# Optimization experiments

Hardware: AMD Instinct MI355X
Metric: run time of the kernel (lower is better)

The kernel has to match this reference:

```python
import jax, jax.numpy as jnp
import numpy as np

N = 32       # number of variables (per-var LSTMs)
L = 128      # window length
D = 128      # hidden dim
HEADS = 8
TAU_MAX = 5
ALPHA = 0.7  # attn_decay_alpha
B = 128      # number of time-ordered windows


def setup_inputs() -> dict:
    key = jax.random.key(0)
    ks = jax.random.split(key, 20)
    s = 0.1
    f = lambda k, shape: (jax.random.normal(k, shape, jnp.float32) * s)
    return {
        "X": jax.random.normal(ks[0], (B, L, N), jnp.float32),
        # per-variable encoder LSTM (input size 1): W_ih (N,4D), W_hh (N,4D,D), combined-style biases kept separate
        "enc_Wih": f(ks[1], (N, 4 * D)),
        "enc_Whh": f(ks[2], (N, 4 * D, D)),
        "enc_b": f(ks[3], (N, 4 * D)),            # b_ih + b_hh merged (mathematically identical)
        "pool_w": f(ks[4], (N, D)),
        "pool_b": f(ks[5], (N,)),
        # shared MultiheadAttention params (torch layout: in_proj (3D,D))
        "in_proj_w": f(ks[6], (3 * D, D)),
        "in_proj_b": f(ks[7], (3 * D,)),
        "out_proj_w": f(ks[8], (D, D)),
        "out_proj_b": f(ks[9], (D,)),
        # per-variable decoder: init_h/init_c Linear(d,d), LSTM(1,d) (input is all-zeros so W_ih drops out), out Linear(d,1)
        "dec_initH_w": f(ks[10], (N, D, D)),
        "dec_initH_b": f(ks[11], (N, D)),
        "dec_initC_w": f(ks[12], (N, D, D)),
        "dec_initC_b": f(ks[13], (N, D)),
        "dec_Whh": f(ks[14], (N, 4 * D, D)),
        "dec_bih": f(ks[15], (N, 4 * D)),
        "dec_bhh": f(ks[16], (N, 4 * D)),
        "dec_out_w": f(ks[17], (N, D)),
        "dec_out_b": f(ks[18], (N,)),
    }


def _lstm_cell(gates, c):
    # torch gate order: i, f, g, o
    i, fg, g, o = jnp.split(gates, 4, axis=-1)
    i = jax.nn.sigmoid(i); fg = jax.nn.sigmoid(fg)
    g = jnp.tanh(g); o = jax.nn.sigmoid(o)
    c = fg * c + i * g
    h = o * jnp.tanh(c)
    return h, c


def _encode(X, Wih, Whh, b, pool_w, pool_b):
    # X: (B,L,N); encoder consumes first L-1 steps of each variable, batched over all N vars
    x = jnp.transpose(X[:, :-1, :], (1, 2, 0))  # (T, N, B)
    Bn = X.shape[0]
    h0 = jnp.zeros((N, Bn, D), X.dtype)

    def step(carry, x_t):  # x_t: (N,B)
        h, c = carry
        gates = (x_t[..., None] * Wih[:, None, :]
                 + jnp.einsum('nbd,ngd->nbg', h, Whh)
                 + b[:, None, :])
        h, c = _lstm_cell(gates, c)
        return (h, c), h

    _, H = jax.lax.scan(step, (h0, h0), x)  # H: (T,N,B,D)
    # TemporalAttnPool: softmax over time of a linear score, weighted sum
    scores = jnp.einsum('tnbd,nd->tnb', H, pool_w) + pool_b[None, :, None]
    a = jax.nn.softmax(scores, axis=0)
    C = jnp.einsum('tnb,tnbd->bnd', a, H)  # (B,N,D)
    return C


def _mha(Q, KV, in_w, in_b, out_w, out_b):
    dh = D // HEADS
    q = Q @ in_w[:D].T + in_b[:D]
    k = KV @ in_w[D:2 * D].T + in_b[D:2 * D]
    v = KV @ in_w[2 * D:].T + in_b[2 * D:]
    sp = lambda x: x.reshape(x.shape[0], x.shape[1], HEADS, dh)
    q, k, v = sp(q), sp(k), sp(v)
    scores = jnp.einsum('bqhd,bkhd->bhqk', q, k) / float(np.sqrt(dh))
    attn = jax.nn.softmax(scores, axis=-1)
    o = jnp.einsum('bhqk,bkhd->bqhd', attn, v).reshape(Q.shape)
    return o @ out_w.T + out_b


def _cross_attend(C, in_w, in_b, out_w, out_b):
    Bn = C.shape[0]
    tmax = min(TAU_MAX, Bn - 1)
    if tmax <= 0:
        return C
    out_sum = jnp.zeros_like(C)
    w_sum = jnp.zeros((Bn, 1, 1), C.dtype)
    for tau in range(1, tmax + 1):  # small fixed loop over lags
        o = _mha(C[tau:], C[:-tau], in_w, in_b, out_w, out_b)
        w = float(np.exp(-ALPHA * (tau - 1)))  # attn_agg == 'decay'
        out_sum = out_sum.at[tau:].add(o * w)
        w_sum = w_sum.at[tau:].add(w)
    out = out_sum / jnp.clip(w_sum, 1e-8)
    return C + out  # residual=True


def _decode(C_star, iHw, iHb, iCw, iCb, Whh, bih, bhh, ow, ob):
    # h0/c0 from tanh(Linear(c_star)); LSTM input is all-zeros so input term reduces to b_ih
    h0 = jnp.tanh(jnp.einsum('bnd,ned->nbe', C_star, iHw) + iHb[:, None, :])
    c0 = jnp.tanh(jnp.einsum('bnd,ned->nbe', C_star, iCw) + iCb[:, None, :])
    b = (bih + bhh)[:, None, :]  # (N,1,4D)

    def step(carry, _):
        h, c = carry
        gates = jnp.einsum('nbd,ngd->nbg', h, Whh) + b
        h, c = _lstm_cell(gates, c)
        o = jnp.einsum('nbd,nd->nb', h, ow) + ob[:, None]
        return (h, c), o

    _, O = jax.lax.scan(step, (h0, c0), None, length=L)  # (L,N,B)
    recon = jnp.transpose(O[:L - 1], (2, 0, 1))  # (B,L-1,N)
    pred = O[L - 1].T                            # (B,N)
    return recon, pred


def reference(X, enc_Wih, enc_Whh, enc_b, pool_w, pool_b,
              in_proj_w, in_proj_b, out_proj_w, out_proj_b,
              dec_initH_w, dec_initH_b, dec_initC_w, dec_initC_b,
              dec_Whh, dec_bih, dec_bhh, dec_out_w, dec_out_b):
    C = _encode(X, enc_Wih, enc_Whh, enc_b, pool_w, pool_b)
    C_star = _cross_attend(C, in_proj_w, in_proj_b, out_proj_w, out_proj_b)
    recon, pred = _decode(C_star, dec_initH_w, dec_initH_b, dec_initC_w, dec_initC_b,
                          dec_Whh, dec_bih, dec_bhh, dec_out_w, dec_out_b)
    return recon, pred, C_star
```

## Files before the change

kernel.cpp:

```cpp
#include <hip/hip_runtime.h>
#include <hip/hip_bf16.h>

typedef unsigned short ushort_t;
typedef unsigned int uint_t;

#define DD   128
#define G4   512
#define BT   16
#define NB   128
#define NV   32

#define OFF_WIH   0
#define OFF_EB    16384
#define OFF_PW    32768
#define OFF_PB    36864
#define OFF_INW   37120
#define OFF_INB   86272
#define OFF_OUTW  86784
#define OFF_OUTB  103168
#define OFF_IHB   103424
#define OFF_ICB   107520
#define OFF_DBIH  111616
#define OFF_DBHH  128000
#define OFF_DOW   144384
#define OFF_DOB   148480
#define P_TOTAL   148736
#define OFF_FLAGS (OFF_PB + 32)

typedef __attribute__((ext_vector_type(8))) short bf16x8;
typedef __attribute__((ext_vector_type(4))) float f32x4;

__device__ __forceinline__ float bf2f(ushort_t u) {
    union { uint_t i; float f; } x; x.i = ((uint_t)u) << 16; return x.f;
}
__device__ __forceinline__ ushort_t f2bf(float f) {
    __hip_bfloat16 h = __float2bfloat16(f);
    return *(ushort_t*)&h;
}
__device__ __forceinline__ uint_t f2u(float f) {
    union { float f; uint_t i; } x; x.f = f; return x.i;
}
__device__ __forceinline__ float u2f(uint_t u) {
    union { uint_t i; float f; } x; x.i = u; return x.f;
}
__device__ __forceinline__ float exp2_f(float x) {
    float r; asm("v_exp_f32 %0, %1" : "=v"(r) : "v"(x)); return r;
}
__device__ __forceinline__ float sigmoid_f(float x) {
    return __builtin_amdgcn_rcpf(1.f + exp2_f(x * -1.442695041f));
}
__device__ __forceinline__ float tanh_f(float x) {
    return 1.f - 2.f * __builtin_amdgcn_rcpf(exp2_f(x * 2.885390082f) + 1.f);
}
__device__ __forceinline__ uint_t cvt_pk_bf16(float a, float b) {
    uint_t r; asm("v_cvt_pk_bf16_f32 %0, %1, %2" : "=v"(r) : "v"(a), "v"(b)); return r;
}
__device__ __forceinline__ bf16x8 pack8(f32x4 a, f32x4 b) {
    union { uint_t u[4]; bf16x8 v; } x;
    x.u[0] = cvt_pk_bf16(a.x, a.y); x.u[1] = cvt_pk_bf16(a.z, a.w);
    x.u[2] = cvt_pk_bf16(b.x, b.y); x.u[3] = cvt_pk_bf16(b.z, b.w);
    return x.v;
}
__device__ __forceinline__ float swz_bcast_l15(float v) {
    return u2f((uint_t)__builtin_amdgcn_ds_swizzle((int)f2u(v), 0x000F));
}
__device__ __forceinline__ void store_out(void* out, long idx, float v, int bf) {
    if (bf) ((ushort_t*)out)[idx] = f2bf(v);
    else    ((float*)out)[idx]    = v;
}
#define LBAR() do { asm volatile("s_waitcnt lgkmcnt(0)" ::: "memory"); \
                    __builtin_amdgcn_s_barrier(); } while (0)

__device__ __forceinline__ int wave_probe(const void* p, int elems) {
    int cap = elems < 2048 ? elems : 2048;
    int lane = threadIdx.x & 63;
    const ushort_t* u = (const ushort_t*)p;
    int cnt = 0, tot = 0;
    for (int j = lane; j < cap; j += 64) {
        ushort_t x = u[j];
        float af = fabsf(bf2f(x));
        tot++;
        if (x == 0 || (af > 1e-7f && af < 100.f)) cnt++;
    }
    #pragma unroll
    for (int off = 32; off >= 1; off >>= 1) {
        cnt += __shfl_xor(cnt, off);
        tot += __shfl_xor(tot, off);
    }
    return (cnt * 10 >= tot * 9) ? 1 : 0;
}

struct Ptr19 { const void* p[19]; };

__global__ __launch_bounds__(256) void prep_kernel(Ptr19 a, float* __restrict__ P,
                                                   float* __restrict__ Xc) {
    __shared__ float tile[32][65];
    if (blockIdx.x < 581) {
        int base = blockIdx.x * 256;
        int src, o0, size;
        if      (base < OFF_EB)   { src = 1;  o0 = base - OFF_WIH;  size = 16384; }
        else if (base < OFF_PW)   { src = 3;  o0 = base - OFF_EB;   size = 16384; }
        else if (base < OFF_PB)   { src = 4;  o0 = base - OFF_PW;   size = 4096;  }
        else if (base < OFF_INW)  { src = 5;  o0 = base - OFF_PB;   size = 32;    }
        else if (base < OFF_INB)  { src = 6;  o0 = base - OFF_INW;  size = 49152; }
        else if (base < OFF_OUTW) { src = 7;  o0 = base - OFF_INB;  size = 384;   }
        else if (base < OFF_OUTB) { src = 8;  o0 = base - OFF_OUTW; size = 16384; }
        else if (base < OFF_IHB)  { src = 9;  o0 = base - OFF_OUTB; size = 128;   }
        else if (base < OFF_ICB)  { src = 11; o0 = base - OFF_IHB;  size = 4096;  }
        else if (base < OFF_DBIH) { src = 13; o0 = base - OFF_ICB;  size = 4096;  }
        else if (base < OFF_DBHH) { src = 15; o0 = base - OFF_DBIH; size = 16384; }
        else if (base < OFF_DOW)  { src = 16; o0 = base - OFF_DBHH; size = 16384; }
        else if (base < OFF_DOB)  { src = 17; o0 = base - OFF_DOW;  size = 4096;  }
        else                      { src = 18; o0 = base - OFF_DOB;  size = 32;    }
        int bf = wave_probe(a.p[src], size);
        int off = o0 + (int)threadIdx.x;
        if (off < size)
            P[base + threadIdx.x] = bf ? bf2f(((const ushort_t*)a.p[src])[off])
                                       : ((const float*)a.p[src])[off];
    } else if (blockIdx.x < 837) {
        int bf = wave_probe(a.p[0], 2048);
        int idx2 = blockIdx.x - 581;
        int bt = (idx2 & 3) * 32, tn0 = (idx2 >> 2) * 64;
        const void* src = a.p[0];
        int tx = threadIdx.x & 63, ty = threadIdx.x >> 6;
        #pragma unroll
        for (int k = 0; k < 8; k++) {
            int row = ty * 8 + k;
            int idx = (bt + row) * 4096 + tn0 + tx;
            tile[row][tx] = bf ? bf2f(((const ushort_t*)src)[idx]) : ((const float*)src)[idx];
        }
        __syncthreads();
        int bx = threadIdx.x & 31, tyy = threadIdx.x >> 5;
        #pragma unroll
        for (int k = 0; k < 8; k++) {
            int tn = tn0 + tyy * 8 + k;
            int t = tn >> 5, nn = tn & 31;
            Xc[t * 4096 + nn * 128 + bt + bx] = tile[bx][tyy * 8 + k];
        }
    } else {
        int which = blockIdx.x - 837;
        int src = (which == 0) ? 0 : (which == 1) ? 2 : (which == 2) ? 10
                : (which == 3) ? 12 : 14;
        int flag = wave_probe(a.p[src], 2048);
        if (threadIdx.x == 0) P[OFF_FLAGS + which] = (float)flag;
    }
}

__global__ __launch_bounds__(512, 2) void enc_kernel(
    const float* __restrict__ Xc, const void* __restrict__ Wraw,
    const float* __restrict__ P, float* __restrict__ Cout)
{
    const int n = blockIdx.y, b0 = blockIdx.x * BT;
    const int tid = threadIdx.x;
    const int w = tid >> 6, lane = tid & 63;
    const int l15 = lane & 15, quad = lane >> 4;
    const int wbf = P[OFF_FLAGS + 1] > 0.5f;
    const int bown = b0 + l15;

    __shared__ alignas(16) ushort_t hS[2][16 * 136];
    for (int i = tid; i < 16 * 136; i += 512) hS[0][i] = 0;

    bf16x8 afrag[4][4];
    #pragma unroll
    for (int typ = 0; typ < 4; typ++) {
        const int g = typ * 128 + 16 * w + l15;
        #pragma unroll
        for (int kc = 0; kc < 4; kc++) {
            const int base = (n * G4 + g) * DD + 32 * kc + 8 * quad;
            if (wbf) {
                afrag[typ][kc] = *(const bf16x8*)((const ushort_t*)Wraw + base);
            } else {
                const float* fp = (const float*)Wraw + base;
                afrag[typ][kc] = pack8(*(const f32x4*)fp, *(const f32x4*)(fp + 4));
            }
        }
    }

    bf16x8 pfrag[4];
    #pragma unroll
    for (int kc = 0; kc < 4; kc++) {
        bf16x8 tmp;
        #pragma unroll
        for (int j = 0; j < 8; j++)
            tmp[j] = (l15 == 0 || l15 == 8)
                   ? (short)f2bf(P[OFF_PW + n * DD + 32 * kc + 8 * quad + j]) : (short)0;
        pfrag[kc] = tmp;
    }

    f32x4 bias4[4], wih4[4];
    #pragma unroll
    for (int typ = 0; typ < 4; typ++) {
        int base = n * G4 + typ * 128 + 16 * w + 4 * quad;
        bias4[typ] = *(const f32x4*)&P[OFF_EB + base];
        wih4[typ]  = *(const f32x4*)&P[OFF_WIH + base];
    }
    const float pb_r = P[OFF_PB + n];
    const f32x4 pb4 = {pb_r, pb_r, pb_r, pb_r};

    float cst[4] = {0.f, 0.f, 0.f, 0.f};
    f32x4 hprev  = {0.f, 0.f, 0.f, 0.f};
    f32x4 hprev2 = {0.f, 0.f, 0.f, 0.f};
    f32x4 Cacc   = {0.f, 0.f, 0.f, 0.f};
    float lR = 0.f, pend = 0.f;

    const float* xnext = Xc + n * 128 + bown;
    float xq = *xnext;
    xnext += 4096;

    if (w & 4) __builtin_amdgcn_s_setprio(1);

#define ENC_STEP(T, RB)                                                              \
    do {                                                                             \
        LBAR();                                                                      \
        bf16x8 bh[4];                                                                \
        _Pragma("unroll")                                                            \
        for (int kc = 0; kc < 4; kc++)                                               \
            bh[kc] = *(const bf16x8*)&hS[RB][l15 * 136 + 32 * kc + 8 * quad];        \
        if ((T) >= 2) {     \
            float e = __expf(pend);                                                  \
            lR += e;                                                                 \
            f32x4 ev = {e, e, e, e};                                                 \
            Cacc += ev * hprev2;                                                     \
        }                                                                            \
        f32x4 xv = {xq, xq, xq, xq};                                                 \
        f32x4 acc[4];                                                                \
        _Pragma("unroll")                                                            \
        for (int typ = 0; typ < 4; typ++)                                            \
            acc[typ] = __builtin_amdgcn_mfma_f32_16x16x32_bf16(                      \
                afrag[typ][0], bh[0], bias4[typ] + xv * wih4[typ], 0, 0, 0);         \
        f32x4 accP = __builtin_amdgcn_mfma_f32_16x16x32_bf16(pfrag[0], bh[0], pb4, 0, 0, 0); \
        xq = *xnext; xnext += 4096;    \
        _Pragma("unroll")                                                            \
        for (int kc = 1; kc < 4; kc++) {                                             \
            accP = __builtin_amdgcn_mfma_f32_16x16x32_bf16(pfrag[kc], bh[kc], accP, 0, 0, 0); \
            _Pragma("unroll")                                                        \
            for (int typ = 0; typ < 4; typ++)                                        \
                acc[typ] = __builtin_amdgcn_mfma_f32_16x16x32_bf16(afrag[typ][kc], bh[kc], acc[typ], 0, 0, 0); \
        }                                                                            \
        if ((T) >= 1) pend = swz_bcast_l15(accP[0]);   \
        float hh[4];                                                                 \
        _Pragma("unroll")                                                            \
        for (int r = 0; r < 4; r++) {                                                \
            float ii = sigmoid_f(acc[0][r]);                                         \
            float ff = sigmoid_f(acc[1][r]);                                         \
            float g2 = tanh_f(acc[2][r]);                                            \
            float oo = sigmoid_f(acc[3][r]);                                         \
            float cc = ff * cst[r] + ii * g2;                                        \
            cst[r] = cc;                                                             \
            hh[r] = oo * tanh_f(cc);                                                 \
        }                                                                            \
        hprev2 = hprev;                                                              \
        hprev.x = hh[0]; hprev.y = hh[1]; hprev.z = hh[2]; hprev.w = hh[3];          \
        uint2 hw;                                                                    \
        hw.x = cvt_pk_bf16(hh[0], hh[1]);                                            \
        hw.y = cvt_pk_bf16(hh[2], hh[3]);                                            \
        *(uint2*)&hS[(RB) ^ 1][l15 * 136 + 16 * w + 4 * quad] = hw;                  \
    } while (0)

    for (int tp = 0; tp < 63; tp++) {
        ENC_STEP(2 * tp, 0);
        ENC_STEP(2 * tp + 1, 1);
    }
    ENC_STEP(126, 0);
#undef ENC_STEP

    LBAR();
    {
        float e = __expf(pend);
        lR += e;
        f32x4 ev = {e, e, e, e};
        Cacc += ev * hprev2;

        f32x4 accP = __builtin_amdgcn_mfma_f32_16x16x32_bf16(
            pfrag[0], *(const bf16x8*)&hS[1][l15 * 136 + 8 * quad], pb4, 0, 0, 0);
        #pragma unroll
        for (int kc = 1; kc < 4; kc++) {
            bf16x8 bh = *(const bf16x8*)&hS[1][l15 * 136 + 32 * kc + 8 * quad];
            accP = __builtin_amdgcn_mfma_f32_16x16x32_bf16(pfrag[kc], bh, accP, 0, 0, 0);
        }
        float e2 = __expf(swz_bcast_l15(accP[0]));
        lR += e2;
        f32x4 ev2 = {e2, e2, e2, e2};
        Cacc += ev2 * hprev;
    }
    float inv = 1.f / lR;
    f32x4 iv = {inv, inv, inv, inv};
    f32x4 cv = Cacc * iv;
    *(f32x4*)&Cout[bown * (NV * DD) + n * DD + 16 * w + 4 * quad] = cv;
}

__global__ __launch_bounds__(256) void qkv_kernel(
    const float* __restrict__ C, const float* __restrict__ P,
    float* __restrict__ q, float* __restrict__ k, float* __restrict__ v)
{
    int b = blockIdx.x, p = blockIdx.y, tid = threadIdx.x;
    int j = tid & 127, half = tid >> 7;
    __shared__ float Cb[NV * DD];
    for (int i = tid; i < NV * DD; i += 256) Cb[i] = C[b * (NV * DD) + i];
    __syncthreads();

    const float* wrow = P + OFF_INW + (p * DD + j) * DD;
    float bias = P[OFF_INB + p * DD + j];
    float acc[16];
    #pragma unroll
    for (int nn = 0; nn < 16; nn++) acc[nn] = bias;

    for (int dc = 0; dc < DD; dc += 8) {
        float4 w0 = *(const float4*)&wrow[dc];
        float4 w1 = *(const float4*)&wrow[dc + 4];
        #pragma unroll
        for (int nn = 0; nn < 16; nn++) {
            const float* cb = &Cb[(half * 16 + nn) * DD + dc];
            float4 c0 = *(float4*)&cb[0];
            float4 c1 = *(float4*)&cb[4];
            acc[nn] += c0.x * w0.x + c0.y * w0.y + c0.z * w0.z + c0.w * w0.w
                     + c1.x * w1.x + c1.y * w1.y + c1.z * w1.z + c1.w * w1.w;
        }
    }
    float* dst = (p == 0) ? q : (p == 1) ? k : v;
    for (int nn = 0; nn < 16; nn++)
        dst[b * (NV * DD) + (half * 16 + nn) * DD + j] = acc[nn];
}

__global__ __launch_bounds__(128) void attn_kernel(
    const float* __restrict__ q, const float* __restrict__ k, const float* __restrict__ v,
    const float* __restrict__ C, const float* __restrict__ P,
    float* __restrict__ Cstar, void* __restrict__ dout)
{
    int b = blockIdx.x, half = blockIdx.y, tid = threadIdx.x;
    int obf = P[OFF_FLAGS + 0] > 0.5f;
    int n0 = half * 16;
    __shared__ float Qs[16 * DD], Ks[NV * DD], Vs[NV * DD];
    float* Os = Ks;
    for (int i = tid; i < 16 * DD; i += 128) Qs[i] = q[b * (NV * DD) + n0 * DD + i];
    __syncthreads();

    int hh = tid >> 4, qi = tid & 15;
    float qreg[16];
    #pragma unroll
    for (int u = 0; u < 4; u++) {
        float4 t4 = *(float4*)&Qs[qi * DD + hh * 16 + 4 * u];
        qreg[4*u] = t4.x; qreg[4*u+1] = t4.y; qreg[4*u+2] = t4.z; qreg[4*u+3] = t4.w;
    }

    float Oacc[16];
    #pragma unroll
    for (int u = 0; u < 16; u++) Oacc[u] = 0.f;
    float wsum = 0.f;
    int tmax = (b < 5) ? b : 5;

    for (int tau = 1; tau <= tmax; tau++) {
        __syncthreads();
        for (int i = tid; i < NV * DD; i += 128) {
            Ks[i] = k[(b - tau) * (NV * DD) + i];
            Vs[i] = v[(b - tau) * (NV * DD) + i];
        }
        __syncthreads();

        float s[NV];
        #pragma unroll
        for (int kk = 0; kk < NV; kk++) {
            float a = 0.f;
            #pragma unroll
            for (int u = 0; u < 4; u++) {
                float4 kv = *(float4*)&Ks[kk * DD + hh * 16 + 4 * u];
                a += qreg[4*u] * kv.x + qreg[4*u+1] * kv.y
                   + qreg[4*u+2] * kv.z + qreg[4*u+3] * kv.w;
            }
            s[kk] = a * 0.25f;
        }
        float mm = s[0];
        #pragma unroll
        for (int kk = 1; kk < NV; kk++) mm = fmaxf(mm, s[kk]);
        float ssum = 0.f;
        #pragma unroll
        for (int kk = 0; kk < NV; kk++) { s[kk] = __expf(s[kk] - mm); ssum += s[kk]; }
        float wdk = __expf(-0.7f * (float)(tau - 1));
        wsum += wdk;
        float wr = wdk / ssum;
        #pragma unroll
        for (int u = 0; u < 4; u++) {
            float ax = 0.f, ay = 0.f, az = 0.f, aw = 0.f;
            #pragma unroll
            for (int kk = 0; kk < NV; kk++) {
                float4 vv = *(float4*)&Vs[kk * DD + hh * 16 + 4 * u];
                ax += s[kk] * vv.x; ay += s[kk] * vv.y;
                az += s[kk] * vv.z; aw += s[kk] * vv.w;
            }
            Oacc[4*u] += wr * ax; Oacc[4*u+1] += wr * ay;
            Oacc[4*u+2] += wr * az; Oacc[4*u+3] += wr * aw;
        }
    }

    __syncthreads();
    float winv = (b > 0) ? 1.f / wsum : 0.f;
    #pragma unroll
    for (int u = 0; u < 16; u++)
        Os[qi * DD + hh * 16 + u] = Oacc[u] * winv;
    __syncthreads();

    int j = tid;
    const float* wrow = P + OFF_OUTW + j * DD;
    float obias = P[OFF_OUTB + j];
    for (int nn = 0; nn < 16; nn++) {
        float a = (b > 0) ? obias : 0.f;
        for (int dc = 0; dc < DD; dc += 8) {
            float4 w0 = *(const float4*)&wrow[dc];
            float4 w1 = *(const float4*)&wrow[dc + 4];
            float4 o0 = *(float4*)&Os[nn * DD + dc];
            float4 o1 = *(float4*)&Os[nn * DD + dc + 4];
            a += o0.x*w0.x + o0.y*w0.y + o0.z*w0.z + o0.w*w0.w
               + o1.x*w1.x + o1.y*w1.y + o1.z*w1.z + o1.w*w1.w;
        }
        int nng = n0 + nn;
        float cs = C[b * (NV * DD) + nng * DD + j] + a;
        Cstar[b * (NV * DD) + nng * DD + j] = cs;
        store_out(dout, 524288 + b * (NV * DD) + nng * DD + j, cs, obf);
    }
}

__global__ __launch_bounds__(512, 2) void dec_kernel(
    const float* __restrict__ Cstar,
    const void* __restrict__ iHw, const void* __restrict__ iCw,
    const void* __restrict__ Wraw,
    const float* __restrict__ P, void* __restrict__ out)
{
    const int n = blockIdx.y, b0 = blockIdx.x * BT;
    const int tid = threadIdx.x;
    const int w = tid >> 6, lane = tid & 63;
    const int l15 = lane & 15, quad = lane >> 4;
    const int obf = P[OFF_FLAGS + 0] > 0.5f;
    const int hbf = P[OFF_FLAGS + 2] > 0.5f;
    const int cbf = P[OFF_FLAGS + 3] > 0.5f;
    const int wbf = P[OFF_FLAGS + 4] > 0.5f;
    const int bown = b0 + l15;

    __shared__ alignas(16) ushort_t hS[2][16 * 136];

    bf16x8 cstB[4];
    #pragma unroll
    for (int kc = 0; kc < 4; kc++) {
        const float* cp = &Cstar[bown * (NV * DD) + n * DD + 32 * kc + 8 * quad];
        cstB[kc] = pack8(*(const f32x4*)&cp[0], *(const f32x4*)&cp[4]);
    }
    float cst[4];
    {
        f32x4 hAcc = *(const f32x4*)&P[OFF_IHB + n * DD + 16 * w + 4 * quad];
        f32x4 cAcc = *(const f32x4*)&P[OFF_ICB + n * DD + 16 * w + 4 * quad];
        #pragma unroll
        for (int kc = 0; kc < 4; kc++) {
            const int base = (n * DD + 16 * w + l15) * DD + 32 * kc + 8 * quad;
            bf16x8 wA;
            if (hbf) wA = *(const bf16x8*)((const ushort_t*)iHw + base);
            else {
                const float* fp = (const float*)iHw + base;
                wA = pack8(*(const f32x4*)fp, *(const f32x4*)(fp + 4));
            }
            hAcc = __builtin_amdgcn_mfma_f32_16x16x32_bf16(wA, cstB[kc], hAcc, 0, 0, 0);
            if (cbf) wA = *(const bf16x8*)((const ushort_t*)iCw + base);
            else {
                const float* fp = (const float*)iCw + base;
                wA = pack8(*(const f32x4*)fp, *(const f32x4*)(fp + 4));
            }
            cAcc = __builtin_amdgcn_mfma_f32_16x16x32_bf16(wA, cstB[kc], cAcc, 0, 0, 0);
        }
        float h0 = tanh_f(hAcc[0]), h1 = tanh_f(hAcc[1]);
        float h2 = tanh_f(hAcc[2]), h3 = tanh_f(hAcc[3]);
        #pragma unroll
        for (int r = 0; r < 4; r++) cst[r] = tanh_f(cAcc[r]);
        uint2 hw;
        hw.x = cvt_pk_bf16(h0, h1);
        hw.y = cvt_pk_bf16(h2, h3);
        *(uint2*)&hS[0][l15 * 136 + 16 * w + 4 * quad] = hw;
    }

    bf16x8 afrag[4][4];
    #pragma unroll
    for (int typ = 0; typ < 4; typ++) {
        const int g = typ * 128 + 16 * w + l15;
        #pragma unroll
        for (int kc = 0; kc < 4; kc++) {
            const int base = (n * G4 + g) * DD + 32 * kc + 8 * quad;
            if (wbf) {
                afrag[typ][kc] = *(const bf16x8*)((const ushort_t*)Wraw + base);
            } else {
                const float* fp = (const float*)Wraw + base;
                afrag[typ][kc] = pack8(*(const f32x4*)fp, *(const f32x4*)(fp + 4));
            }
        }
    }

    bf16x8 pfrag[4];
    #pragma unroll
    for (int kc = 0; kc < 4; kc++) {
        bf16x8 tmp;
        #pragma unroll
        for (int j = 0; j < 8; j++)
            tmp[j] = (l15 == 0) ? (short)f2bf(P[OFF_DOW + n * DD + 32 * kc + 8 * quad + j]) : (short)0;
        pfrag[kc] = tmp;
    }

    f32x4 bias4[4];
    #pragma unroll
    for (int typ = 0; typ < 4; typ++) {
        int base = n * G4 + typ * 128 + 16 * w + 4 * quad;
        f32x4 b1 = *(const f32x4*)&P[OFF_DBIH + base];
        f32x4 b2 = *(const f32x4*)&P[OFF_DBHH + base];
        bias4[typ] = b1 + b2;
    }
    const float ob_r = P[OFF_DOB + n];
    const f32x4 ob4 = {ob_r, ob_r, ob_r, ob_r};

    if (w & 4) __builtin_amdgcn_s_setprio(1);

#define DEC_STEP(T, RB)                                                              \
    do {                                                                             \
        LBAR();                                                                      \
        bf16x8 bh[4];                                                                \
        _Pragma("unroll")                                                            \
        for (int kc = 0; kc < 4; kc++)                                               \
            bh[kc] = *(const bf16x8*)&hS[RB][l15 * 136 + 32 * kc + 8 * quad];        \
        f32x4 acc[4];                                                                \
        _Pragma("unroll")                                                            \
        for (int typ = 0; typ < 4; typ++)                                            \
            acc[typ] = __builtin_amdgcn_mfma_f32_16x16x32_bf16(afrag[typ][0], bh[0], bias4[typ], 0, 0, 0); \
        _Pragma("unroll")                                                            \
        for (int kc = 1; kc < 4; kc++)                                               \
            _Pragma("unroll")                                                        \
            for (int typ = 0; typ < 4; typ++)                                        \
                acc[typ] = __builtin_amdgcn_mfma_f32_16x16x32_bf16(afrag[typ][kc], bh[kc], acc[typ], 0, 0, 0); \
        if (w == ((T) & 7)) {    \
            f32x4 accP = __builtin_amdgcn_mfma_f32_16x16x32_bf16(pfrag[0], bh[0], ob4, 0, 0, 0); \
            _Pragma("unroll")                                                        \
            for (int kc = 1; kc < 4; kc++)                                           \
                accP = __builtin_amdgcn_mfma_f32_16x16x32_bf16(pfrag[kc], bh[kc], accP, 0, 0, 0); \
            if ((T) > 0 && quad == 0)                                                \
                store_out(out, (long)bown * 4064 + (long)((T) - 1) * NV + n, accP[0], obf); \
        }                                                                            \
        float hh[4];                                                                 \
        _Pragma("unroll")                                                            \
        for (int r = 0; r < 4; r++) {                                                \
            float ii = sigmoid_f(acc[0][r]);                                         \
            float ff = sigmoid_f(acc[1][r]);                                         \
            float g2 = tanh_f(acc[2][r]);                                            \
            float oo = sigmoid_f(acc[3][r]);                                         \
            float cc = ff * cst[r] + ii * g2;                                        \
            cst[r] = cc;                                                             \
            hh[r] = oo * tanh_f(cc);                                                 \
        }                                                                            \
        uint2 hw;                                                                    \
        hw.x = cvt_pk_bf16(hh[0], hh[1]);                                            \
        hw.y = cvt_pk_bf16(hh[2], hh[3]);                                            \
        *(uint2*)&hS[(RB) ^ 1][l15 * 136 + 16 * w + 4 * quad] = hw;                  \
    } while (0)

    for (int tp = 0; tp < 64; tp++) {
        DEC_STEP(2 * tp, 0);
        DEC_STEP(2 * tp + 1, 1);
    }
#undef DEC_STEP

    LBAR();
    if (w == 0) {
        f32x4 accP = __builtin_amdgcn_mfma_f32_16x16x32_bf16(
            pfrag[0], *(const bf16x8*)&hS[0][l15 * 136 + 8 * quad], ob4, 0, 0, 0);
        #pragma unroll
        for (int kc = 1; kc < 4; kc++) {
            bf16x8 bh = *(const bf16x8*)&hS[0][l15 * 136 + 32 * kc + 8 * quad];
            accP = __builtin_amdgcn_mfma_f32_16x16x32_bf16(pfrag[kc], bh, accP, 0, 0, 0);
        }
        if (quad == 0)
            store_out(out, 520192 + (long)bown * NV + n, accP[0], obf);
    }
}

extern "C" void kernel_launch(void* const* d_in, const int* in_sizes, int n_in,
                              void* d_out, int out_size, void* d_ws, size_t ws_size,
                              hipStream_t stream) {
    char* ws = (char*)d_ws;
    float*    P    = (float*)(ws + 0);
    float*    Xc   = (float*)(ws + (1u << 20));
    float*    C    = (float*)(ws + (3u << 20));
    float*    qb   = (float*)(ws + (5u << 20));
    float*    kb   = (float*)(ws + (7u << 20));
    float*    vb   = (float*)(ws + (9u << 20));
    float*    Cst  = (float*)(ws + (11u << 20));

    Ptr19 a;
    for (int i = 0; i < 19; i++) a.p[i] = d_in[i];

    prep_kernel<<<842, 256, 0, stream>>>(a, P, Xc);
    enc_kernel<<<dim3(8, 32), 512, 0, stream>>>(Xc, d_in[2], P, C);
    qkv_kernel<<<dim3(128, 3), 256, 0, stream>>>(C, P, qb, kb, vb);
    attn_kernel<<<dim3(128, 2), 128, 0, stream>>>(qb, kb, vb, C, P, Cst, d_out);
    dec_kernel<<<dim3(8, 32), 512, 0, stream>>>(Cst, d_in[10], d_in[12], d_in[14], P, d_out);
}
```

Baseline: 416.7 us.

## Prefetch next K/V window into registers and drop encoder h-history copies

The attention kernel now loads the next tau's K and V blocks into registers as float4 while the current tau is being computed, replacing scalar global-to-shared copies with vectorised register staging. This is meant to hide global load latency behind the score and softmax math. In the encoder, the two-step h history is kept in a ping-pong array indexed by the shared-memory buffer instead of being shifted each step, which removes register moves. The dtype probe also samples half as many elements. The cost is extra register pressure from the 16 float4 prefetch registers and a less robust dtype detection.

```diff
diff --git a/kernel.cpp b/kernel.cpp
--- a/kernel.cpp
+++ b/kernel.cpp
@@ -72,7 +72,7 @@
                     __builtin_amdgcn_s_barrier(); } while (0)
 
 __device__ __forceinline__ int wave_probe(const void* p, int elems) {
-    int cap = elems < 2048 ? elems : 2048;
+    int cap = elems < 1024 ? elems : 1024;
     int lane = threadIdx.x & 63;
     const ushort_t* u = (const ushort_t*)p;
     int cnt = 0, tot = 0;
@@ -118,7 +118,7 @@
             P[base + threadIdx.x] = bf ? bf2f(((const ushort_t*)a.p[src])[off])
                                        : ((const float*)a.p[src])[off];
     } else if (blockIdx.x < 837) {
-        int bf = wave_probe(a.p[0], 2048);
+        int bf = wave_probe(a.p[0], 1024);
         int idx2 = blockIdx.x - 581;
         int bt = (idx2 & 3) * 32, tn0 = (idx2 >> 2) * 64;
         const void* src = a.p[0];
@@ -141,7 +141,7 @@
         int which = blockIdx.x - 837;
         int src = (which == 0) ? 0 : (which == 1) ? 2 : (which == 2) ? 10
                 : (which == 3) ? 12 : 14;
-        int flag = wave_probe(a.p[src], 2048);
+        int flag = wave_probe(a.p[src], 1024);
         if (threadIdx.x == 0) P[OFF_FLAGS + which] = (float)flag;
     }
 }
@@ -198,8 +198,9 @@
     const f32x4 pb4 = {pb_r, pb_r, pb_r, pb_r};
 
     float cst[4] = {0.f, 0.f, 0.f, 0.f};
-    f32x4 hprev  = {0.f, 0.f, 0.f, 0.f};
-    f32x4 hprev2 = {0.f, 0.f, 0.f, 0.f};
+    f32x4 hpair[2];
+    hpair[0] = f32x4{0.f, 0.f, 0.f, 0.f};
+    hpair[1] = f32x4{0.f, 0.f, 0.f, 0.f};
     f32x4 Cacc   = {0.f, 0.f, 0.f, 0.f};
     float lR = 0.f, pend = 0.f;
 
@@ -216,11 +217,11 @@
         _Pragma("unroll")                                                            \
         for (int kc = 0; kc < 4; kc++)                                               \
             bh[kc] = *(const bf16x8*)&hS[RB][l15 * 136 + 32 * kc + 8 * quad];        \
-        if ((T) >= 2) {     \
+        if ((T) >= 2) {         \
             float e = __expf(pend);                                                  \
             lR += e;                                                                 \
             f32x4 ev = {e, e, e, e};                                                 \
-            Cacc += ev * hprev2;                                                     \
+            Cacc += ev * hpair[RB];                                                  \
         }                                                                            \
         f32x4 xv = {xq, xq, xq, xq};                                                 \
         f32x4 acc[4];                                                                \
@@ -249,8 +250,8 @@
             cst[r] = cc;                                                             \
             hh[r] = oo * tanh_f(cc);                                                 \
         }                                                                            \
-        hprev2 = hprev;                                                              \
-        hprev.x = hh[0]; hprev.y = hh[1]; hprev.z = hh[2]; hprev.w = hh[3];          \
+        hpair[RB].x = hh[0]; hpair[RB].y = hh[1];                                    \
+        hpair[RB].z = hh[2]; hpair[RB].w = hh[3];                                    \
         uint2 hw;                                                                    \
         hw.x = cvt_pk_bf16(hh[0], hh[1]);                                            \
         hw.y = cvt_pk_bf16(hh[2], hh[3]);                                            \
@@ -269,7 +270,7 @@
         float e = __expf(pend);
         lR += e;
         f32x4 ev = {e, e, e, e};
-        Cacc += ev * hprev2;
+        Cacc += ev * hpair[1];
 
         f32x4 accP = __builtin_amdgcn_mfma_f32_16x16x32_bf16(
             pfrag[0], *(const bf16x8*)&hS[1][l15 * 136 + 8 * quad], pb4, 0, 0, 0);
@@ -281,7 +282,7 @@
         float e2 = __expf(swz_bcast_l15(accP[0]));
         lR += e2;
         f32x4 ev2 = {e2, e2, e2, e2};
-        Cacc += ev2 * hprev;
+        Cacc += ev2 * hpair[0];
     }
     float inv = 1.f / lR;
     f32x4 iv = {inv, inv, inv, inv};
@@ -349,13 +350,29 @@
     float wsum = 0.f;
     int tmax = (b < 5) ? b : 5;
 
+    float4 kr[8], vr[8];
+#define ATT_LOAD(TAU)                                                            \
+    do {                                                                         \
+        const float4* kp = (const float4*)&k[(b - (TAU)) * (NV * DD)];           \
+        const float4* vp = (const float4*)&v[(b - (TAU)) * (NV * DD)];           \
+        _Pragma("unroll")                                                        \
+        for (int u = 0; u < 8; u++) {                                            \
+            kr[u] = kp[tid + 128 * u];                                           \
+            vr[u] = vp[tid + 128 * u];                                           \
+        }                                                                        \
+    } while (0)
+
+    if (tmax >= 1) ATT_LOAD(1);
+
     for (int tau = 1; tau <= tmax; tau++) {
         __syncthreads();
-        for (int i = tid; i < NV * DD; i += 128) {
-            Ks[i] = k[(b - tau) * (NV * DD) + i];
-            Vs[i] = v[(b - tau) * (NV * DD) + i];
+        #pragma unroll
+        for (int u = 0; u < 8; u++) {
+            ((float4*)Ks)[tid + 128 * u] = kr[u];
+            ((float4*)Vs)[tid + 128 * u] = vr[u];
         }
         __syncthreads();
+        if (tau < tmax) ATT_LOAD(tau + 1);
 
         float s[NV];
         #pragma unroll
@@ -391,6 +408,7 @@
             Oacc[4*u+2] += wr * az; Oacc[4*u+3] += wr * aw;
         }
     }
+#undef ATT_LOAD
 
     __syncthreads();
     float winv = (b > 0) ? 1.f / wsum : 0.f;
```

Measured after the change: 419.2 us. Within noise of the previous version (+0.6%).
